# Kernel optimization log

Hardware: AMD Instinct MI355X
Metric: run time of the kernel (lower is better)

Reference implementation:

```python
import jax, jax.numpy as jnp
import numpy as np

T, D_IN, D, H, A = 8192, 2048, 512, 512, 18  # seq_len, obs_dim, dense_size, cell_size, action_size


def setup_inputs() -> dict:
    key = jax.random.key(0)
    ks = jax.random.split(key, 12)
    g = lambda k, sh, s: (jax.random.normal(k, sh, jnp.float32) * s)
    return {
        "x": g(ks[0], (T, D_IN), 1.0),
        "prev_hidden": jnp.zeros((1, H), jnp.float32),
        "W1": g(ks[1], (D_IN, D), 0.02), "b1": jnp.zeros((D,), jnp.float32),
        "W2": g(ks[2], (D, D), 0.04),    "b2": jnp.zeros((D,), jnp.float32),
        "Wg": g(ks[3], (D, 3 * H), 0.04),   # GRU input kernel [D, 3H] (z|r|h)
        "Ug": g(ks[4], (H, 3 * H), 0.04),   # GRU recurrent kernel [H, 3H]
        "bg": jnp.zeros((2, 3 * H), jnp.float32),  # reset_after=True: input + recurrent bias
        "Wp": g(ks[5], (H, A), 0.05), "bp": jnp.zeros((A,), jnp.float32),
        "Wv": g(ks[6], (H, 1), 0.05), "bv": jnp.zeros((1,), jnp.float32),
    }


def reference(x, prev_hidden, W1, b1, W2, b2, Wg, Ug, bg, Wp, bp, Wv, bv):
    # MLP front-end (relu)
    z = jax.nn.relu(x @ W1 + b1)
    z = jax.nn.relu(z @ W2 + b2)
    # Precompute input projections for all timesteps: [T, 3H]
    X = z @ Wg + bg[0]
    b_rec = bg[1]

    def step(h, xt):  # h: [1,H], xt: [3H]
        rec = h @ Ug + b_rec                    # [1, 3H]
        xz, xr, xh = jnp.split(xt, 3)           # each [H]
        rz, rr, rh = jnp.split(rec, 3, axis=1)  # each [1, H]
        zt = jax.nn.sigmoid(xz + rz)
        rt = jax.nn.sigmoid(xr + rr)
        hh = jax.nn.sigmoid(xh + rt * rh)       # activation='sigmoid' (candidate)
        hn = zt * h + (1.0 - zt) * hh
        return hn, hn[0]

    hT, seq = jax.lax.scan(step, prev_hidden, X)  # seq: [T, H]
    policy = jax.nn.softmax(seq @ Wp + bp, axis=-1)
    value = seq @ Wv + bv
    return policy, value, hT
```

## Files before the change

kernel.cpp:

```cpp
#include <hip/hip_runtime.h>
#include <hip/hip_bf16.h>


#define T_STEPS 8192
#define DIN 2048
#define DD 512
#define HHH 512
#define AACT 18
#define H3 1536
#define NWG 32

typedef __attribute__((ext_vector_type(8))) short short8;
typedef __attribute__((ext_vector_type(4))) float f32x4;

__global__ void cast_f32_bf16(const float* __restrict__ in,
                              __hip_bfloat16* __restrict__ out, int n)
{
    int i = blockIdx.x * 256 + threadIdx.x;
    if (i < n) out[i] = __float2bfloat16(in[i]);
}

__global__ void init_ctl(int* ctl) { ctl[0] = 0; ctl[1] = 0; ctl[2] = 0; }

__global__ __launch_bounds__(256) void gemm_bf16(
    const float* __restrict__ A32, const __hip_bfloat16* __restrict__ A16,
    const __hip_bfloat16* __restrict__ B, const float* __restrict__ bias,
    __hip_bfloat16* __restrict__ Cb, float* __restrict__ Cf,
    int M, int N, int K, int relu)
{
    const int m0 = blockIdx.x * 64;
    const int n0 = blockIdx.y * 64;
    const int t  = threadIdx.x;
    const int wave = t >> 6;
    const int lane = t & 63;
    const int quad = lane >> 4;
    const int l16  = lane & 15;

    __shared__ __align__(16) __hip_bfloat16 As[64 * 40];
    __shared__ __align__(16) __hip_bfloat16 Bs[64 * 40];

    f32x4 acc[4];
#pragma unroll
    for (int c = 0; c < 4; ++c) acc[c] = (f32x4){0.f, 0.f, 0.f, 0.f};

    const int ar = t >> 2, akc = (t & 3) * 8;
    const int bk = t >> 3, bn  = (t & 7) * 8;

    for (int kb = 0; kb < K; kb += 32) {
        if (A32) {
            const float* src = A32 + (size_t)(m0 + ar) * K + kb + akc;
            float4 f0 = *(const float4*)(src);
            float4 f1 = *(const float4*)(src + 4);
            union { short8 v; __hip_bfloat16 h[8]; } u;
            u.h[0] = __float2bfloat16(f0.x); u.h[1] = __float2bfloat16(f0.y);
            u.h[2] = __float2bfloat16(f0.z); u.h[3] = __float2bfloat16(f0.w);
            u.h[4] = __float2bfloat16(f1.x); u.h[5] = __float2bfloat16(f1.y);
            u.h[6] = __float2bfloat16(f1.z); u.h[7] = __float2bfloat16(f1.w);
            *(short8*)&As[ar * 40 + akc] = u.v;
        } else {
            const __hip_bfloat16* src = A16 + (size_t)(m0 + ar) * K + kb + akc;
            *(short8*)&As[ar * 40 + akc] = *(const short8*)src;
        }
        {
            const __hip_bfloat16* src = B + (size_t)(kb + bk) * N + n0 + bn;
            short8 v = *(const short8*)src;
            const __hip_bfloat16* vh = (const __hip_bfloat16*)&v;
#pragma unroll
            for (int i = 0; i < 8; ++i) Bs[(bn + i) * 40 + bk] = vh[i];
        }
        __syncthreads();

        short8 a = *(const short8*)&As[(wave * 16 + l16) * 40 + quad * 8];
#pragma unroll
        for (int c = 0; c < 4; ++c) {
            short8 b = *(const short8*)&Bs[(c * 16 + l16) * 40 + quad * 8];
            acc[c] = __builtin_amdgcn_mfma_f32_16x16x32_bf16(a, b, acc[c], 0, 0, 0);
        }
        __syncthreads();
    }

#pragma unroll
    for (int c = 0; c < 4; ++c) {
        const int col = n0 + c * 16 + l16;
        const float bb = bias ? bias[col] : 0.f;
#pragma unroll
        for (int r = 0; r < 4; ++r) {
            const int row = m0 + wave * 16 + quad * 4 + r;
            float v = acc[c][r] + bb;
            if (relu) v = fmaxf(v, 0.f);
            if (Cb) Cb[(size_t)row * N + col] = __float2bfloat16(v);
            if (Cf) Cf[(size_t)row * N + col] = v;
        }
    }
}

template <int CTRL>
__device__ __forceinline__ float dpp_red_add(float x)
{
    int sh = __builtin_amdgcn_update_dpp(0, __float_as_int(x), CTRL, 0xF, 0xF, true);
    return x + __int_as_float(sh);
}

__global__ __launch_bounds__(256)
__attribute__((amdgpu_waves_per_eu(1, 1)))
void scan_kernel(
    const float* __restrict__ X,
    const float* __restrict__ Ug,
    const float* __restrict__ bg,
    const float* __restrict__ h0,
    float* __restrict__ seq,
    unsigned long long* __restrict__ hbuf,
    float* __restrict__ hT,
    int* __restrict__ ctl)
{
    const int t  = threadIdx.x;
    const int wg = blockIdx.x;
    const int jl = t >> 4;
    const int kp = t & 15;
    const int j  = wg * 16 + jl;
    const int k0 = kp * 32;

    __shared__ __align__(16) float h_lds[2][16 * 36];
    __shared__ int wg_abort;
    if (t == 0) wg_abort = 0;

    float wz[32], wr[32], wh[32];
#pragma unroll
    for (int m = 0; m < 32; ++m) {
        const float* row = Ug + (size_t)(k0 + m) * H3;
        wz[m] = row[j];
        wr[m] = row[512 + j];
        wh[m] = row[1024 + j];
    }
#pragma unroll
    for (int m = 0; m < 32; ++m) {
        asm volatile("" : "+a"(wz[m]), "+a"(wr[m]), "+a"(wh[m]));
    }

    const float* brec = bg + H3;
    const float bz = brec[j], brr = brec[512 + j], bh = brec[1024 + j];
    float hj = h0[j];

    const int k1 = t, k2 = t + 256;
    const int a1 = (k1 >> 5) * 36 + (k1 & 31);
    const int a2 = (k2 >> 5) * 36 + (k2 & 31);

    float xz = 0.f, xr = 0.f, xh = 0.f;
    if (kp == 0) { xz = X[j]; xr = X[512 + j]; xh = X[1024 + j]; }

    for (int s = 0; s < T_STEPS; ++s) {
        float* hl = h_lds[s & 1];

        float nxz = 0.f, nxr = 0.f, nxh = 0.f;
        if (kp == 0 && s + 1 < T_STEPS) {
            const float* Xs = X + (size_t)(s + 1) * H3;
            nxz = Xs[j]; nxr = Xs[512 + j]; nxh = Xs[1024 + j];
        }

        if (s == 0) {
            hl[a1] = h0[k1];
            hl[a2] = h0[k2];
        } else {
            const unsigned long long* src = hbuf + ((size_t)(s & 1) << 9);
            unsigned long long v1 = __hip_atomic_load(src + k1, __ATOMIC_RELAXED, __HIP_MEMORY_SCOPE_AGENT);
            unsigned long long v2 = __hip_atomic_load(src + k2, __ATOMIC_RELAXED, __HIP_MEMORY_SCOPE_AGENT);
            bool ok1 = (unsigned)(v1 >> 32) == (unsigned)s;
            bool ok2 = (unsigned)(v2 >> 32) == (unsigned)s;
            int guard = 0;
            while (!(ok1 && ok2)) {
                if (!ok1) v1 = __hip_atomic_load(src + k1, __ATOMIC_RELAXED, __HIP_MEMORY_SCOPE_AGENT);
                if (!ok2) v2 = __hip_atomic_load(src + k2, __ATOMIC_RELAXED, __HIP_MEMORY_SCOPE_AGENT);
                ok1 = (unsigned)(v1 >> 32) == (unsigned)s;
                ok2 = (unsigned)(v2 >> 32) == (unsigned)s;
                if ((++guard & 1023) == 0) {
                    int ab = __hip_atomic_load(ctl + 2, __ATOMIC_RELAXED,
                                               __HIP_MEMORY_SCOPE_AGENT);
                    if (ab || guard > (1 << 16)) {
                        wg_abort = 1;
                        __hip_atomic_store(ctl + 2, 1, __ATOMIC_RELAXED,
                                           __HIP_MEMORY_SCOPE_AGENT);
                        break;
                    }
                }
            }
            hl[a1] = __uint_as_float((unsigned)v1);
            hl[a2] = __uint_as_float((unsigned)v2);
        }
        __syncthreads();
        if (wg_abort) return;

        float accz = 0.f, accr = 0.f, acch = 0.f;
        const float* hb = &hl[kp * 36];
#pragma unroll
        for (int m = 0; m < 32; m += 4) {
            float4 hv = *(const float4*)(hb + m);
            accz = fmaf(hv.x, wz[m    ], accz);
            accz = fmaf(hv.y, wz[m + 1], accz);
            accz = fmaf(hv.z, wz[m + 2], accz);
            accz = fmaf(hv.w, wz[m + 3], accz);
            accr = fmaf(hv.x, wr[m    ], accr);
            accr = fmaf(hv.y, wr[m + 1], accr);
            accr = fmaf(hv.z, wr[m + 2], accr);
            accr = fmaf(hv.w, wr[m + 3], accr);
            acch = fmaf(hv.x, wh[m    ], acch);
            acch = fmaf(hv.y, wh[m + 1], acch);
            acch = fmaf(hv.z, wh[m + 2], acch);
            acch = fmaf(hv.w, wh[m + 3], acch);
        }
        accz = dpp_red_add<0x108>(accz);
        accr = dpp_red_add<0x108>(accr);
        acch = dpp_red_add<0x108>(acch);
        accz = dpp_red_add<0x104>(accz);
        accr = dpp_red_add<0x104>(accr);
        acch = dpp_red_add<0x104>(acch);
        accz = dpp_red_add<0x102>(accz);
        accr = dpp_red_add<0x102>(accr);
        acch = dpp_red_add<0x102>(acch);
        accz = dpp_red_add<0x101>(accz);
        accr = dpp_red_add<0x101>(accr);
        acch = dpp_red_add<0x101>(acch);

        if (kp == 0) {
            const float rz = accz + bz, rr = accr + brr, rh = acch + bh;
            const float zt = 1.f / (1.f + __expf(-(xz + rz)));
            const float rt = 1.f / (1.f + __expf(-(xr + rr)));
            const float hc = 1.f / (1.f + __expf(-(xh + rt * rh)));
            const float hn = zt * hj + (1.f - zt) * hc;
            hj = hn;
            unsigned long long pk =
                ((unsigned long long)(unsigned)(s + 1) << 32) | (unsigned)__float_as_uint(hn);
            __hip_atomic_store(hbuf + (size_t)(((s + 1) & 1) << 9) + j, pk,
                               __ATOMIC_RELAXED, __HIP_MEMORY_SCOPE_AGENT);
            seq[(size_t)s * HHH + j] = hn;
            if (s == T_STEPS - 1) hT[j] = hn;
        }
        xz = nxz; xr = nxr; xh = nxh;
    }
}

__global__ __launch_bounds__(64) void heads_kernel(
    const float* __restrict__ seq, const float* __restrict__ Wp,
    const float* __restrict__ bp, const float* __restrict__ Wv,
    const float* __restrict__ bv, float* __restrict__ pol,
    float* __restrict__ val)
{
    const int s = blockIdx.x;
    const int l = threadIdx.x;
    const float* h = seq + (size_t)s * HHH;

    float acc[19];
#pragma unroll
    for (int jj = 0; jj < 19; ++jj) acc[jj] = 0.f;

#pragma unroll
    for (int kk = 0; kk < 8; ++kk) {
        const int k = kk * 64 + l;
        const float hv = h[k];
        const float* wrow = Wp + (size_t)k * AACT;
#pragma unroll
        for (int jj = 0; jj < AACT; ++jj) acc[jj] = fmaf(hv, wrow[jj], acc[jj]);
        acc[18] = fmaf(hv, Wv[k], acc[18]);
    }
#pragma unroll
    for (int jj = 0; jj < 19; ++jj) {
        float v = acc[jj];
#pragma unroll
        for (int off = 32; off; off >>= 1) v += __shfl_down(v, off, 64);
        acc[jj] = v;
    }
    if (l == 0) {
        float lg[18], mx = -1e30f;
#pragma unroll
        for (int jj = 0; jj < AACT; ++jj) { lg[jj] = acc[jj] + bp[jj]; mx = fmaxf(mx, lg[jj]); }
        float sum = 0.f;
#pragma unroll
        for (int jj = 0; jj < AACT; ++jj) { lg[jj] = __expf(lg[jj] - mx); sum += lg[jj]; }
        const float inv = 1.f / sum;
#pragma unroll
        for (int jj = 0; jj < AACT; ++jj) pol[(size_t)s * AACT + jj] = lg[jj] * inv;
        val[s] = acc[18] + bv[0];
    }
}

extern "C" void kernel_launch(void* const* d_in, const int* in_sizes, int n_in,
                              void* d_out, int out_size, void* d_ws, size_t ws_size,
                              hipStream_t stream)
{
    const float* x  = (const float*)d_in[0];
    const float* h0 = (const float*)d_in[1];
    const float* W1 = (const float*)d_in[2];
    const float* b1 = (const float*)d_in[3];
    const float* W2 = (const float*)d_in[4];
    const float* b2 = (const float*)d_in[5];
    const float* Wg = (const float*)d_in[6];
    const float* Ug = (const float*)d_in[7];
    const float* bg = (const float*)d_in[8];
    const float* Wp = (const float*)d_in[9];
    const float* bp = (const float*)d_in[10];
    const float* Wv = (const float*)d_in[11];
    const float* bv = (const float*)d_in[12];

    char* ws = (char*)d_ws;
    __hip_bfloat16* W1b = (__hip_bfloat16*)(ws + 0);
    __hip_bfloat16* W2b = (__hip_bfloat16*)(ws + 2097152);
    __hip_bfloat16* Wgb = (__hip_bfloat16*)(ws + 2621440);
    __hip_bfloat16* z1b = (__hip_bfloat16*)(ws + 4194304);
    __hip_bfloat16* z2b = (__hip_bfloat16*)(ws + 12582912);
    float*          Xb  = (float*)(ws + 20971520);
    float*          seq = (float*)(ws + 71303168);
    unsigned long long* hbuf = (unsigned long long*)(ws + 88080384);
    int* ctl = (int*)(ws + 4194304);

    float* out = (float*)d_out;
    float* pol = out;
    float* val = out + (size_t)T_STEPS * AACT;
    float* hT  = out + (size_t)T_STEPS * AACT + T_STEPS;

    cast_f32_bf16<<<DIN * DD / 256, 256, 0, stream>>>(W1, W1b, DIN * DD);
    cast_f32_bf16<<<DD * DD / 256, 256, 0, stream>>>(W2, W2b, DD * DD);
    cast_f32_bf16<<<DD * H3 / 256, 256, 0, stream>>>(Wg, Wgb, DD * H3);

    dim3 blk(256);
    gemm_bf16<<<dim3(T_STEPS / 64, DD / 64), blk, 0, stream>>>(
        x, nullptr, W1b, b1, z1b, nullptr, T_STEPS, DD, DIN, 1);
    gemm_bf16<<<dim3(T_STEPS / 64, DD / 64), blk, 0, stream>>>(
        nullptr, z1b, W2b, b2, z2b, nullptr, T_STEPS, DD, DD, 1);
    gemm_bf16<<<dim3(T_STEPS / 64, H3 / 64), blk, 0, stream>>>(
        nullptr, z2b, Wgb, bg, nullptr, Xb, T_STEPS, H3, DD, 0);

    init_ctl<<<1, 1, 0, stream>>>(ctl);
    scan_kernel<<<NWG, 256, 0, stream>>>(Xb, Ug, bg, h0, seq, hbuf, hT, ctl);

    heads_kernel<<<T_STEPS, 64, 0, stream>>>(seq, Wp, bp, Wv, bv, pol, val);
}
```

Measured before the change: 12.40 ms.

## Replace per-step block barrier with per-wave private h staging

Each wave now polls all 512 hidden values itself (8 per lane) and writes them into its own LDS staging buffer. This removes the per-timestep __syncthreads across the four waves of the workgroup, so each wave only waits for its own data. In exchange every wave issues four times as many global atomic loads per step and uses more LDS. Abort handling becomes per-wave via __any and a volatile flag.

```diff
diff --git a/kernel.cpp b/kernel.cpp
--- a/kernel.cpp
+++ b/kernel.cpp
@@ -113,16 +113,19 @@
     float* __restrict__ hT,
     int* __restrict__ ctl)
 {
-    const int t  = threadIdx.x;
-    const int wg = blockIdx.x;
-    const int jl = t >> 4;
-    const int kp = t & 15;
-    const int j  = wg * 16 + jl;
-    const int k0 = kp * 32;
-
-    __shared__ __align__(16) float h_lds[2][16 * 36];
+    const int t    = threadIdx.x;
+    const int wg   = blockIdx.x;
+    const int wave = t >> 6;
+    const int l    = t & 63;
+    const int jl   = t >> 4;
+    const int kp   = t & 15;
+    const int j    = wg * 16 + jl;
+    const int k0   = kp * 32;
+
+    __shared__ __align__(16) float hstage[4][16 * 36];
     __shared__ int wg_abort;
     if (t == 0) wg_abort = 0;
+    __syncthreads();
 
     float wz[32], wr[32], wh[32];
 #pragma unroll
@@ -141,15 +144,70 @@
     const float bz = brec[j], brr = brec[512 + j], bh = brec[1024 + j];
     float hj = h0[j];
 
-    const int k1 = t, k2 = t + 256;
-    const int a1 = (k1 >> 5) * 36 + (k1 & 31);
-    const int a2 = (k2 >> 5) * 36 + (k2 & 31);
+    float* const hw = hstage[wave];
+    float* const wbase = hw + (l >> 2) * 36 + 8 * (l & 3);
+    const int slot0 = l * 8;
 
     float xz = 0.f, xr = 0.f, xh = 0.f;
     if (kp == 0) { xz = X[j]; xr = X[512 + j]; xh = X[1024 + j]; }
 
     for (int s = 0; s < T_STEPS; ++s) {
-        float* hl = h_lds[s & 1];
+        if (s == 0) {
+            float4 a = *(const float4*)(h0 + slot0);
+            float4 b = *(const float4*)(h0 + slot0 + 4);
+            *(float2*)(wbase + 0) = make_float2(a.x, a.y);
+            *(float2*)(wbase + 2) = make_float2(a.z, a.w);
+            *(float2*)(wbase + 4) = make_float2(b.x, b.y);
+            *(float2*)(wbase + 6) = make_float2(b.z, b.w);
+        } else {
+            const unsigned long long* src = hbuf + ((size_t)(s & 1) << 9) + slot0;
+            unsigned long long v[8];
+            bool ok[8];
+#pragma unroll
+            for (int i = 0; i < 8; ++i) {
+                v[i] = __hip_atomic_load(src + i, __ATOMIC_RELAXED, __HIP_MEMORY_SCOPE_AGENT);
+                ok[i] = false;
+            }
+            int guard = 0;
+            bool bail = false;
+            for (;;) {
+                bool all = true;
+#pragma unroll
+                for (int i = 0; i < 8; ++i) {
+                    if (!ok[i]) {
+                        if ((unsigned)(v[i] >> 32) == (unsigned)s) ok[i] = true;
+                        else all = false;
+                    }
+                }
+                if (all) break;
+#pragma unroll
+                for (int i = 0; i < 8; ++i)
+                    if (!ok[i]) v[i] = __hip_atomic_load(src + i, __ATOMIC_RELAXED, __HIP_MEMORY_SCOPE_AGENT);
+                if ((++guard & 1023) == 0) {
+                    int ab = __hip_atomic_load(ctl + 2, __ATOMIC_RELAXED,
+                                               __HIP_MEMORY_SCOPE_AGENT);
+                    if (ab || *(volatile int*)&wg_abort || guard > (1 << 16)) {
+                        bail = true;
+                        break;
+                    }
+                }
+            }
+            if (__any(bail)) {
+                *(volatile int*)&wg_abort = 1;
+                if (l == 0)
+                    __hip_atomic_store(ctl + 2, 1, __ATOMIC_RELAXED,
+                                       __HIP_MEMORY_SCOPE_AGENT);
+                return;
+            }
+            *(float2*)(wbase + 0) = make_float2(__uint_as_float((unsigned)v[0]),
+                                                __uint_as_float((unsigned)v[1]));
+            *(float2*)(wbase + 2) = make_float2(__uint_as_float((unsigned)v[2]),
+                                                __uint_as_float((unsigned)v[3]));
+            *(float2*)(wbase + 4) = make_float2(__uint_as_float((unsigned)v[4]),
+                                                __uint_as_float((unsigned)v[5]));
+            *(float2*)(wbase + 6) = make_float2(__uint_as_float((unsigned)v[6]),
+                                                __uint_as_float((unsigned)v[7]));
+        }
 
         float nxz = 0.f, nxr = 0.f, nxh = 0.f;
         if (kp == 0 && s + 1 < T_STEPS) {
@@ -157,40 +215,11 @@
             nxz = Xs[j]; nxr = Xs[512 + j]; nxh = Xs[1024 + j];
         }
 
-        if (s == 0) {
-            hl[a1] = h0[k1];
-            hl[a2] = h0[k2];
-        } else {
-            const unsigned long long* src = hbuf + ((size_t)(s & 1) << 9);
-            unsigned long long v1 = __hip_atomic_load(src + k1, __ATOMIC_RELAXED, __HIP_MEMORY_SCOPE_AGENT);
-            unsigned long long v2 = __hip_atomic_load(src + k2, __ATOMIC_RELAXED, __HIP_MEMORY_SCOPE_AGENT);
-            bool ok1 = (unsigned)(v1 >> 32) == (unsigned)s;
-            bool ok2 = (unsigned)(v2 >> 32) == (unsigned)s;
-            int guard = 0;
-            while (!(ok1 && ok2)) {
-                if (!ok1) v1 = __hip_atomic_load(src + k1, __ATOMIC_RELAXED, __HIP_MEMORY_SCOPE_AGENT);
-                if (!ok2) v2 = __hip_atomic_load(src + k2, __ATOMIC_RELAXED, __HIP_MEMORY_SCOPE_AGENT);
-                ok1 = (unsigned)(v1 >> 32) == (unsigned)s;
-                ok2 = (unsigned)(v2 >> 32) == (unsigned)s;
-                if ((++guard & 1023) == 0) {
-                    int ab = __hip_atomic_load(ctl + 2, __ATOMIC_RELAXED,
-                                               __HIP_MEMORY_SCOPE_AGENT);
-                    if (ab || guard > (1 << 16)) {
-                        wg_abort = 1;
-                        __hip_atomic_store(ctl + 2, 1, __ATOMIC_RELAXED,
-                                           __HIP_MEMORY_SCOPE_AGENT);
-                        break;
-                    }
-                }
-            }
-            hl[a1] = __uint_as_float((unsigned)v1);
-            hl[a2] = __uint_as_float((unsigned)v2);
-        }
-        __syncthreads();
-        if (wg_abort) return;
+        asm volatile("s_waitcnt lgkmcnt(0)" ::: "memory");
+        __builtin_amdgcn_sched_barrier(0);
 
         float accz = 0.f, accr = 0.f, acch = 0.f;
-        const float* hb = &hl[kp * 36];
+        const float* hb = hw + kp * 36;
 #pragma unroll
         for (int m = 0; m < 32; m += 4) {
             float4 hv = *(const float4*)(hb + m);
```

Result: slower. 36.68 ms (+195.9%).
